# Optimization experiments

Measured on AMD Instinct MI355X. Metric: run time of the kernel, lower is better.

Reference implementation:

```python
import jax, jax.numpy as jnp
import numpy as np

N_QUBITS = 8
N_LAYERS = 2


def _ry(theta):
    # theta: (B,) -> (B, 2, 2) complex64 RY matrices
    c = jnp.cos(theta / 2)
    s = jnp.sin(theta / 2)
    m = jnp.stack([jnp.stack([c, -s], -1), jnp.stack([s, c], -1)], -2)
    return m.astype(jnp.complex64)


def _rx(theta):
    # theta: scalar -> (2, 2) complex64 RX matrix
    c = jnp.cos(theta / 2).astype(jnp.complex64)
    js = (-1j * jnp.sin(theta / 2)).astype(jnp.complex64)
    return jnp.stack([jnp.stack([c, js], -1), jnp.stack([js, c], -1)], -2)


def _apply_1q(state, gate, wire):
    # state: (B, 2,...,2); gate: (B,2,2) per-sample or (2,2) shared
    s = jnp.moveaxis(state, 1 + wire, -1)
    if gate.ndim == 3:
        s = jnp.einsum('b...a,bca->b...c', s, gate)
    else:
        s = jnp.einsum('...a,ca->...c', s, gate)
    return jnp.moveaxis(s, -1, 1 + wire)


def _cnot(state, ctrl, tgt):
    # flip target axis on the control=1 slice
    s = jnp.moveaxis(state, (1 + ctrl, 1 + tgt), (1, 2))
    s = jnp.stack([s[:, 0], jnp.flip(s[:, 1], axis=1)], axis=1)
    return jnp.moveaxis(s, (1, 2), (1 + ctrl, 1 + tgt))


def setup_inputs() -> dict:
    key = jax.random.key(0)
    k1, k2 = jax.random.split(key)
    inputs = jax.random.normal(k1, (65536, N_QUBITS), dtype=jnp.float32)
    weights = jax.random.normal(k2, (N_LAYERS, N_QUBITS), dtype=jnp.float32) * 0.1
    return {"inputs": inputs, "weights": weights}


def reference(inputs, weights):
    B = inputs.shape[0]
    # |0...0> statevector, axis 1+i corresponds to wire i (PennyLane ordering)
    state = jnp.zeros((B,) + (2,) * N_QUBITS, dtype=jnp.complex64)
    state = state.at[(slice(None),) + (0,) * N_QUBITS].set(1.0)
    # Encoding: RY(inputs[:, i]) on wire i (per-sample angles)
    for i in range(N_QUBITS):
        state = _apply_1q(state, _ry(inputs[:, i]), i)
    # Variational layers: CNOT chain + RX(weights[layer, i])
    for layer in range(N_LAYERS):
        for i in range(N_QUBITS - 1):
            state = _cnot(state, i, i + 1)
        for i in range(N_QUBITS):
            state = _apply_1q(state, _rx(weights[layer, i]), i)
    probs = jnp.abs(state) ** 2  # (B, 2,...,2) real
    outs = []
    for i in range(N_QUBITS):
        axes = tuple(a for a in range(1, N_QUBITS + 1) if a != 1 + i)
        p = probs.sum(axes)  # (B, 2)
        outs.append(p[:, 0] - p[:, 1])  # <Z_i>
    return jnp.stack(outs, axis=-1).astype(jnp.float32)
```

## Files before the change

### kernel.cpp

```cpp
#include <hip/hip_runtime.h>


constexpr int NQ = 8;

__global__ __launch_bounds__(256) void vqc_closed(
    const float* __restrict__ inputs,
    const float* __restrict__ weights,
    float* __restrict__ out,
    int B)
{
    const int t = blockIdx.x * 256 + threadIdx.x;
    if (t >= B) return;

    const float4 a4 = ((const float4*)(inputs + (size_t)t * NQ))[0];
    const float4 b4 = ((const float4*)(inputs + (size_t)t * NQ))[1];
    const float xx[8] = {a4.x, a4.y, a4.z, a4.w, b4.x, b4.y, b4.z, b4.w};
    float sx[8], cx[8];
#pragma unroll
    for (int w = 0; w < 8; ++w) __sincosf(xx[w], &sx[w], &cx[w]);

    float sA[8], cA[8], sB[8], cB[8];
#pragma unroll
    for (int w = 0; w < 8; ++w) __sincosf(weights[w], &sA[w], &cA[w]);
#pragma unroll
    for (int w = 0; w < 8; ++w) __sincosf(weights[8 + w], &sB[w], &cB[w]);

    const float pA01 = cA[0]*cA[1], qA01 = sA[0]*sA[1];
    const float pA23 = cA[2]*cA[3], qA23 = sA[2]*sA[3];
    const float pA45 = cA[4]*cA[5], qA45 = sA[4]*sA[5];
    const float pA12 = cA[1]*cA[2], qA12 = sA[1]*sA[2];
    const float pA34 = cA[3]*cA[4], qA34 = sA[3]*sA[4];
    const float E7 = cA[6]*(cA[7]*cB[7] - sA[7]*sB[7]);
    const float O7 = -sA[6]*(sA[7]*cB[7] + cA[7]*sB[7]);

    const float z0 = cx[0]*(cA[0]*cB[0] - sA[0]*sB[0]*sx[1]*sx[2]);

    const float z1 = cx[1]*( cA[0]*cA[1]*cB[1]
                   - sA[0]*sA[1]*cB[1]*sx[0]*sx[2]
                   - sA[0]*cA[1]*sB[1]*sx[0]*sx[3]
                   - cA[0]*sA[1]*sB[1]*sx[2]*sx[3] );

    const float z2 = cx[0]*cx[2]*cA[0]*( cA[1]*cA[2]*cB[2]
                   - sA[1]*sA[2]*cB[2]*sx[1]*sx[3]
                   - sA[1]*cA[2]*sB[2]*sx[1]*sx[4]
                   - cA[1]*sA[2]*sB[2]*sx[3]*sx[4] );

    const float z3 = cx[1]*cx[3]*(
          pA01*( cA[2]*cA[3]*cB[3]
               - sA[2]*sA[3]*cB[3]*sx[2]*sx[4]
               - sA[2]*cA[3]*sB[3]*sx[2]*sx[5]
               - cA[2]*sA[3]*sB[3]*sx[4]*sx[5] )
        - qA01*( cA[2]*cA[3]*cB[3]*sx[0]*sx[2]
               - sA[2]*sA[3]*cB[3]*sx[0]*sx[4]
               - sA[2]*cA[3]*sB[3]*sx[0]*sx[5]
               - cA[2]*sA[3]*sB[3]*sx[0]*sx[2]*sx[4]*sx[5] ) );

    const float z4 = cx[0]*cx[2]*cx[4]*cA[0]*(
          pA12*( cA[3]*cA[4]*cB[4]
               - sA[3]*sA[4]*cB[4]*sx[3]*sx[5]
               - sA[3]*cA[4]*sB[4]*sx[3]*sx[6]
               - cA[3]*sA[4]*sB[4]*sx[5]*sx[6] )
        - qA12*( cA[3]*cA[4]*cB[4]*sx[1]*sx[3]
               - sA[3]*sA[4]*cB[4]*sx[1]*sx[5]
               - sA[3]*cA[4]*sB[4]*sx[1]*sx[6]
               - cA[3]*sA[4]*sB[4]*sx[1]*sx[3]*sx[5]*sx[6] ) );

    const float z5 = cx[1]*cx[3]*cx[5]*(
          pA01*( pA23*( cA[4]*cA[5]*cB[5]
                      - sA[4]*sA[5]*cB[5]*sx[4]*sx[6]
                      - sA[4]*cA[5]*sB[5]*sx[4]*sx[7]
                      - cA[4]*sA[5]*sB[5]*sx[6]*sx[7] )
              - qA23*( cA[4]*cA[5]*cB[5]*sx[2]*sx[4]
                      - sA[4]*sA[5]*cB[5]*sx[2]*sx[6]
                      - sA[4]*cA[5]*sB[5]*sx[2]*sx[7]
                      - cA[4]*sA[5]*sB[5]*sx[2]*sx[4]*sx[6]*sx[7] ) )
        - qA01*( pA23*( cA[4]*cA[5]*cB[5]*sx[0]*sx[2]
                      - sA[4]*sA[5]*cB[5]*sx[0]*sx[2]*sx[4]*sx[6]
                      - sA[4]*cA[5]*sB[5]*sx[0]*sx[2]*sx[4]*sx[7]
                      - cA[4]*sA[5]*sB[5]*sx[0]*sx[2]*sx[6]*sx[7] )
              - qA23*( cA[4]*cA[5]*cB[5]*sx[0]*sx[4]
                      - sA[4]*sA[5]*cB[5]*sx[0]*sx[6]
                      - sA[4]*cA[5]*sB[5]*sx[0]*sx[7]
                      - cA[4]*sA[5]*sB[5]*sx[0]*sx[4]*sx[6]*sx[7] ) ) );

    const float z6 = cx[0]*cx[2]*cx[4]*cx[6]*cA[0]*(
          pA12*( pA34*( cA[5]*cA[6]*cB[6]
                      - sA[5]*sA[6]*cB[6]*sx[5]*sx[7]
                      - sA[5]*cA[6]*sB[6]*sx[5]
                      - cA[5]*sA[6]*sB[6]*sx[7] )
              - qA34*( cA[5]*cA[6]*cB[6]*sx[3]*sx[5]
                      - sA[5]*sA[6]*cB[6]*sx[3]*sx[7]
                      - sA[5]*cA[6]*sB[6]*sx[3]
                      - cA[5]*sA[6]*sB[6]*sx[3]*sx[5]*sx[7] ) )
        - qA12*( pA34*( cA[5]*cA[6]*cB[6]*sx[1]*sx[3]
                      - sA[5]*sA[6]*cB[6]*sx[1]*sx[3]*sx[5]*sx[7]
                      - sA[5]*cA[6]*sB[6]*sx[1]*sx[3]*sx[5]
                      - cA[5]*sA[6]*sB[6]*sx[1]*sx[3]*sx[7] )
              - qA34*( cA[5]*cA[6]*cB[6]*sx[1]*sx[5]
                      - sA[5]*sA[6]*cB[6]*sx[1]*sx[7]
                      - sA[5]*cA[6]*sB[6]*sx[1]
                      - cA[5]*sA[6]*sB[6]*sx[1]*sx[5]*sx[7] ) ) );

    const float z7 = cx[1]*cx[3]*cx[5]*cx[7]*(
          pA01*( pA23*( pA45*( E7 + O7*sx[6] )
                      - qA45*( E7*sx[4]*sx[6] + O7*sx[4] ) )
              - qA23*( pA45*( E7*sx[2]*sx[4] + O7*sx[2]*sx[4]*sx[6] )
                      - qA45*( E7*sx[2]*sx[6] + O7*sx[2] ) ) )
        - qA01*( pA23*( pA45*( E7*sx[0]*sx[2] + O7*sx[0]*sx[2]*sx[6] )
                      - qA45*( E7*sx[0]*sx[2]*sx[4]*sx[6] + O7*sx[0]*sx[2]*sx[4] ) )
              - qA23*( pA45*( E7*sx[0]*sx[4] + O7*sx[0]*sx[4]*sx[6] )
                      - qA45*( E7*sx[0]*sx[6] + O7*sx[0] ) ) ) );

    float4* o = (float4*)(out + (size_t)t * NQ);
    o[0] = make_float4(z0, z1, z2, z3);
    o[1] = make_float4(z4, z5, z6, z7);
}

extern "C" void kernel_launch(void* const* d_in, const int* in_sizes, int n_in,
                              void* d_out, int out_size, void* d_ws, size_t ws_size,
                              hipStream_t stream) {
    const float* inputs  = (const float*)d_in[0];
    const float* weights = (const float*)d_in[1];
    float* out = (float*)d_out;
    const int B = in_sizes[0] / NQ;
    const int blocks = (B + 255) / 256;
    vqc_closed<<<blocks, 256, 0, stream>>>(inputs, weights, out, B);
}
```

Before: 9.784 us.

## Split output qubits across two threads per sample and share weight trig via LDS

Each sample is now handled by two threads. One computes the even-indexed expectation values and the other the odd ones, which doubles the thread count and halves per-thread arithmetic. The 16 weight sin/cos values are computed once per block by 16 threads and read from shared memory, so every thread no longer recomputes them. In exchange, both threads reload and recompute the input sincos. Output is written as scalar strided stores instead of float4, and a block-wide barrier is added.

```diff
diff --git a/kernel.cpp b/kernel.cpp
--- a/kernel.cpp
+++ b/kernel.cpp
@@ -3,117 +3,138 @@
 
 constexpr int NQ = 8;
 
-__global__ __launch_bounds__(256) void vqc_closed(
+__global__ __launch_bounds__(256) void vqc_closed2(
     const float* __restrict__ inputs,
     const float* __restrict__ weights,
     float* __restrict__ out,
     int B)
 {
-    const int t = blockIdx.x * 256 + threadIdx.x;
-    if (t >= B) return;
+    __shared__ float W[32];
 
-    const float4 a4 = ((const float4*)(inputs + (size_t)t * NQ))[0];
-    const float4 b4 = ((const float4*)(inputs + (size_t)t * NQ))[1];
+    const int tb = threadIdx.x;
+    if (tb < 16) {
+        float ss, cc;
+        __sincosf(weights[tb], &ss, &cc);
+        const int base = (tb >> 3) << 4;
+        const int off  = tb & 7;
+        W[base + off]     = cc;
+        W[base + 8 + off] = ss;
+    }
+    __syncthreads();
+
+    const int sl     = tb & 127;
+    const int u      = tb >> 7;
+    const int sample = blockIdx.x * 128 + sl;
+    if (sample >= B) return;
+
+    const float4 a4 = ((const float4*)(inputs + (size_t)sample * NQ))[0];
+    const float4 b4 = ((const float4*)(inputs + (size_t)sample * NQ))[1];
     const float xx[8] = {a4.x, a4.y, a4.z, a4.w, b4.x, b4.y, b4.z, b4.w};
     float sx[8], cx[8];
 #pragma unroll
     for (int w = 0; w < 8; ++w) __sincosf(xx[w], &sx[w], &cx[w]);
 
-    float sA[8], cA[8], sB[8], cB[8];
+    float cA[8], sA[8], cB[8], sB[8];
 #pragma unroll
-    for (int w = 0; w < 8; ++w) __sincosf(weights[w], &sA[w], &cA[w]);
-#pragma unroll
-    for (int w = 0; w < 8; ++w) __sincosf(weights[8 + w], &sB[w], &cB[w]);
+    for (int j = 0; j < 8; ++j) {
+        cA[j] = W[j];      sA[j] = W[8 + j];
+        cB[j] = W[16 + j]; sB[j] = W[24 + j];
+    }
 
-    const float pA01 = cA[0]*cA[1], qA01 = sA[0]*sA[1];
-    const float pA23 = cA[2]*cA[3], qA23 = sA[2]*sA[3];
-    const float pA45 = cA[4]*cA[5], qA45 = sA[4]*sA[5];
-    const float pA12 = cA[1]*cA[2], qA12 = sA[1]*sA[2];
-    const float pA34 = cA[3]*cA[4], qA34 = sA[3]*sA[4];
-    const float E7 = cA[6]*(cA[7]*cB[7] - sA[7]*sB[7]);
-    const float O7 = -sA[6]*(sA[7]*cB[7] + cA[7]*sB[7]);
+    float* o = out + (size_t)sample * NQ;
 
-    const float z0 = cx[0]*(cA[0]*cB[0] - sA[0]*sB[0]*sx[1]*sx[2]);
+    if (u == 0) {
+        const float pA12 = cA[1]*cA[2], qA12 = sA[1]*sA[2];
+        const float pA34 = cA[3]*cA[4], qA34 = sA[3]*sA[4];
 
-    const float z1 = cx[1]*( cA[0]*cA[1]*cB[1]
-                   - sA[0]*sA[1]*cB[1]*sx[0]*sx[2]
-                   - sA[0]*cA[1]*sB[1]*sx[0]*sx[3]
-                   - cA[0]*sA[1]*sB[1]*sx[2]*sx[3] );
+        const float z0 = cx[0]*(cA[0]*cB[0] - sA[0]*sB[0]*sx[1]*sx[2]);
 
-    const float z2 = cx[0]*cx[2]*cA[0]*( cA[1]*cA[2]*cB[2]
-                   - sA[1]*sA[2]*cB[2]*sx[1]*sx[3]
-                   - sA[1]*cA[2]*sB[2]*sx[1]*sx[4]
-                   - cA[1]*sA[2]*sB[2]*sx[3]*sx[4] );
+        const float z2 = cx[0]*cx[2]*cA[0]*( cA[1]*cA[2]*cB[2]
+                       - sA[1]*sA[2]*cB[2]*sx[1]*sx[3]
+                       - sA[1]*cA[2]*sB[2]*sx[1]*sx[4]
+                       - cA[1]*sA[2]*sB[2]*sx[3]*sx[4] );
 
-    const float z3 = cx[1]*cx[3]*(
-          pA01*( cA[2]*cA[3]*cB[3]
-               - sA[2]*sA[3]*cB[3]*sx[2]*sx[4]
-               - sA[2]*cA[3]*sB[3]*sx[2]*sx[5]
-               - cA[2]*sA[3]*sB[3]*sx[4]*sx[5] )
-        - qA01*( cA[2]*cA[3]*cB[3]*sx[0]*sx[2]
-               - sA[2]*sA[3]*cB[3]*sx[0]*sx[4]
-               - sA[2]*cA[3]*sB[3]*sx[0]*sx[5]
-               - cA[2]*sA[3]*sB[3]*sx[0]*sx[2]*sx[4]*sx[5] ) );
+        const float z4 = cx[0]*cx[2]*cx[4]*cA[0]*(
+              pA12*( cA[3]*cA[4]*cB[4]
+                   - sA[3]*sA[4]*cB[4]*sx[3]*sx[5]
+                   - sA[3]*cA[4]*sB[4]*sx[3]*sx[6]
+                   - cA[3]*sA[4]*sB[4]*sx[5]*sx[6] )
+            - qA12*( cA[3]*cA[4]*cB[4]*sx[1]*sx[3]
+                   - sA[3]*sA[4]*cB[4]*sx[1]*sx[5]
+                   - sA[3]*cA[4]*sB[4]*sx[1]*sx[6]
+                   - cA[3]*sA[4]*sB[4]*sx[1]*sx[3]*sx[5]*sx[6] ) );
 
-    const float z4 = cx[0]*cx[2]*cx[4]*cA[0]*(
-          pA12*( cA[3]*cA[4]*cB[4]
-               - sA[3]*sA[4]*cB[4]*sx[3]*sx[5]
-               - sA[3]*cA[4]*sB[4]*sx[3]*sx[6]
-               - cA[3]*sA[4]*sB[4]*sx[5]*sx[6] )
-        - qA12*( cA[3]*cA[4]*cB[4]*sx[1]*sx[3]
-               - sA[3]*sA[4]*cB[4]*sx[1]*sx[5]
-               - sA[3]*cA[4]*sB[4]*sx[1]*sx[6]
-               - cA[3]*sA[4]*sB[4]*sx[1]*sx[3]*sx[5]*sx[6] ) );
+        const float z6 = cx[0]*cx[2]*cx[4]*cx[6]*cA[0]*(
+              pA12*( pA34*( cA[5]*cA[6]*cB[6]
+                          - sA[5]*sA[6]*cB[6]*sx[5]*sx[7]
+                          - sA[5]*cA[6]*sB[6]*sx[5]
+                          - cA[5]*sA[6]*sB[6]*sx[7] )
+                  - qA34*( cA[5]*cA[6]*cB[6]*sx[3]*sx[5]
+                          - sA[5]*sA[6]*cB[6]*sx[3]*sx[7]
+                          - sA[5]*cA[6]*sB[6]*sx[3]
+                          - cA[5]*sA[6]*sB[6]*sx[3]*sx[5]*sx[7] ) )
+            - qA12*( pA34*( cA[5]*cA[6]*cB[6]*sx[1]*sx[3]
+                          - sA[5]*sA[6]*cB[6]*sx[1]*sx[3]*sx[5]*sx[7]
+                          - sA[5]*cA[6]*sB[6]*sx[1]*sx[3]*sx[5]
+                          - cA[5]*sA[6]*sB[6]*sx[1]*sx[3]*sx[7] )
+                  - qA34*( cA[5]*cA[6]*cB[6]*sx[1]*sx[5]
+                          - sA[5]*sA[6]*cB[6]*sx[1]*sx[7]
+                          - sA[5]*cA[6]*sB[6]*sx[1]
+                          - cA[5]*sA[6]*sB[6]*sx[1]*sx[5]*sx[7] ) ) );
 
-    const float z5 = cx[1]*cx[3]*cx[5]*(
-          pA01*( pA23*( cA[4]*cA[5]*cB[5]
-                      - sA[4]*sA[5]*cB[5]*sx[4]*sx[6]
-                      - sA[4]*cA[5]*sB[5]*sx[4]*sx[7]
-                      - cA[4]*sA[5]*sB[5]*sx[6]*sx[7] )
-              - qA23*( cA[4]*cA[5]*cB[5]*sx[2]*sx[4]
-                      - sA[4]*sA[5]*cB[5]*sx[2]*sx[6]
-                      - sA[4]*cA[5]*sB[5]*sx[2]*sx[7]
-                      - cA[4]*sA[5]*sB[5]*sx[2]*sx[4]*sx[6]*sx[7] ) )
-        - qA01*( pA23*( cA[4]*cA[5]*cB[5]*sx[0]*sx[2]
-                      - sA[4]*sA[5]*cB[5]*sx[0]*sx[2]*sx[4]*sx[6]
-                      - sA[4]*cA[5]*sB[5]*sx[0]*sx[2]*sx[4]*sx[7]
-                      - cA[4]*sA[5]*sB[5]*sx[0]*sx[2]*sx[6]*sx[7] )
-              - qA23*( cA[4]*cA[5]*cB[5]*sx[0]*sx[4]
-                      - sA[4]*sA[5]*cB[5]*sx[0]*sx[6]
-                      - sA[4]*cA[5]*sB[5]*sx[0]*sx[7]
-                      - cA[4]*sA[5]*sB[5]*sx[0]*sx[4]*sx[6]*sx[7] ) ) );
+        o[0] = z0; o[2] = z2; o[4] = z4; o[6] = z6;
+    } else {
+        const float pA01 = cA[0]*cA[1], qA01 = sA[0]*sA[1];
+        const float pA23 = cA[2]*cA[3], qA23 = sA[2]*sA[3];
+        const float pA45 = cA[4]*cA[5], qA45 = sA[4]*sA[5];
+        const float E7 = cA[6]*(cA[7]*cB[7] - sA[7]*sB[7]);
+        const float O7 = -sA[6]*(sA[7]*cB[7] + cA[7]*sB[7]);
 
-    const float z6 = cx[0]*cx[2]*cx[4]*cx[6]*cA[0]*(
-          pA12*( pA34*( cA[5]*cA[6]*cB[6]
-                      - sA[5]*sA[6]*cB[6]*sx[5]*sx[7]
-                      - sA[5]*cA[6]*sB[6]*sx[5]
-                      - cA[5]*sA[6]*sB[6]*sx[7] )
-              - qA34*( cA[5]*cA[6]*cB[6]*sx[3]*sx[5]
-                      - sA[5]*sA[6]*cB[6]*sx[3]*sx[7]
-                      - sA[5]*cA[6]*sB[6]*sx[3]
-                      - cA[5]*sA[6]*sB[6]*sx[3]*sx[5]*sx[7] ) )
-        - qA12*( pA34*( cA[5]*cA[6]*cB[6]*sx[1]*sx[3]
-                      - sA[5]*sA[6]*cB[6]*sx[1]*sx[3]*sx[5]*sx[7]
-                      - sA[5]*cA[6]*sB[6]*sx[1]*sx[3]*sx[5]
-                      - cA[5]*sA[6]*sB[6]*sx[1]*sx[3]*sx[7] )
-              - qA34*( cA[5]*cA[6]*cB[6]*sx[1]*sx[5]
-                      - sA[5]*sA[6]*cB[6]*sx[1]*sx[7]
-                      - sA[5]*cA[6]*sB[6]*sx[1]
-                      - cA[5]*sA[6]*sB[6]*sx[1]*sx[5]*sx[7] ) ) );
+        const float z1 = cx[1]*( cA[0]*cA[1]*cB[1]
+                       - sA[0]*sA[1]*cB[1]*sx[0]*sx[2]
+                       - sA[0]*cA[1]*sB[1]*sx[0]*sx[3]
+                       - cA[0]*sA[1]*sB[1]*sx[2]*sx[3] );
 
-    const float z7 = cx[1]*cx[3]*cx[5]*cx[7]*(
-          pA01*( pA23*( pA45*( E7 + O7*sx[6] )
-                      - qA45*( E7*sx[4]*sx[6] + O7*sx[4] ) )
-              - qA23*( pA45*( E7*sx[2]*sx[4] + O7*sx[2]*sx[4]*sx[6] )
-                      - qA45*( E7*sx[2]*sx[6] + O7*sx[2] ) ) )
-        - qA01*( pA23*( pA45*( E7*sx[0]*sx[2] + O7*sx[0]*sx[2]*sx[6] )
-                      - qA45*( E7*sx[0]*sx[2]*sx[4]*sx[6] + O7*sx[0]*sx[2]*sx[4] ) )
-              - qA23*( pA45*( E7*sx[0]*sx[4] + O7*sx[0]*sx[4]*sx[6] )
-                      - qA45*( E7*sx[0]*sx[6] + O7*sx[0] ) ) ) );
+        const float z3 = cx[1]*cx[3]*(
+              pA01*( cA[2]*cA[3]*cB[3]
+                   - sA[2]*sA[3]*cB[3]*sx[2]*sx[4]
+                   - sA[2]*cA[3]*sB[3]*sx[2]*sx[5]
+                   - cA[2]*sA[3]*sB[3]*sx[4]*sx[5] )
+            - qA01*( cA[2]*cA[3]*cB[3]*sx[0]*sx[2]
+                   - sA[2]*sA[3]*cB[3]*sx[0]*sx[4]
+                   - sA[2]*cA[3]*sB[3]*sx[0]*sx[5]
+                   - cA[2]*sA[3]*sB[3]*sx[0]*sx[2]*sx[4]*sx[5] ) );
 
-    float4* o = (float4*)(out + (size_t)t * NQ);
-    o[0] = make_float4(z0, z1, z2, z3);
-    o[1] = make_float4(z4, z5, z6, z7);
+        const float z5 = cx[1]*cx[3]*cx[5]*(
+              pA01*( pA23*( cA[4]*cA[5]*cB[5]
+                          - sA[4]*sA[5]*cB[5]*sx[4]*sx[6]
+                          - sA[4]*cA[5]*sB[5]*sx[4]*sx[7]
+                          - cA[4]*sA[5]*sB[5]*sx[6]*sx[7] )
+                  - qA23*( cA[4]*cA[5]*cB[5]*sx[2]*sx[4]
+                          - sA[4]*sA[5]*cB[5]*sx[2]*sx[6]
+                          - sA[4]*cA[5]*sB[5]*sx[2]*sx[7]
+                          - cA[4]*sA[5]*sB[5]*sx[2]*sx[4]*sx[6]*sx[7] ) )
+            - qA01*( pA23*( cA[4]*cA[5]*cB[5]*sx[0]*sx[2]
+                          - sA[4]*sA[5]*cB[5]*sx[0]*sx[2]*sx[4]*sx[6]
+                          - sA[4]*cA[5]*sB[5]*sx[0]*sx[2]*sx[4]*sx[7]
+                          - cA[4]*sA[5]*sB[5]*sx[0]*sx[2]*sx[6]*sx[7] )
+                  - qA23*( cA[4]*cA[5]*cB[5]*sx[0]*sx[4]
+                          - sA[4]*sA[5]*cB[5]*sx[0]*sx[6]
+                          - sA[4]*cA[5]*sB[5]*sx[0]*sx[7]
+                          - cA[4]*sA[5]*sB[5]*sx[0]*sx[4]*sx[6]*sx[7] ) ) );
+
+        const float z7 = cx[1]*cx[3]*cx[5]*cx[7]*(
+              pA01*( pA23*( pA45*( E7 + O7*sx[6] )
+                          - qA45*( E7*sx[4]*sx[6] + O7*sx[4] ) )
+                  - qA23*( pA45*( E7*sx[2]*sx[4] + O7*sx[2]*sx[4]*sx[6] )
+                          - qA45*( E7*sx[2]*sx[6] + O7*sx[2] ) ) )
+            - qA01*( pA23*( pA45*( E7*sx[0]*sx[2] + O7*sx[0]*sx[2]*sx[6] )
+                          - qA45*( E7*sx[0]*sx[2]*sx[4]*sx[6] + O7*sx[0]*sx[2]*sx[4] ) )
+                  - qA23*( pA45*( E7*sx[0]*sx[4] + O7*sx[0]*sx[4]*sx[6] )
+                          - qA45*( E7*sx[0]*sx[6] + O7*sx[0] ) ) ) );
+
+        o[1] = z1; o[3] = z3; o[5] = z5; o[7] = z7;
+    }
 }
 
 extern "C" void kernel_launch(void* const* d_in, const int* in_sizes, int n_in,
@@ -123,6 +144,6 @@
     const float* weights = (const float*)d_in[1];
     float* out = (float*)d_out;
     const int B = in_sizes[0] / NQ;
-    const int blocks = (B + 255) / 256;
-    vqc_closed<<<blocks, 256, 0, stream>>>(inputs, weights, out, B);
+    const int blocks = (B + 127) / 128;
+    vqc_closed2<<<blocks, 256, 0, stream>>>(inputs, weights, out, B);
 }
```

After: 10.52 us. 7.5% more time.
